# Kernel tuning notes

Measured on AMD Instinct MI355X. Metric: run time of the kernel, lower is better.

The kernel has to match this reference:

```python
import jax, jax.numpy as jnp
import numpy as np

IN_DIM = 128
NUM_IDX = 128
LATENT = 512
FF_HID = 4 * IN_DIM
EPS = 1e-5


def _layernorm(x, g, b):
    mu = jnp.mean(x, axis=-1, keepdims=True)
    var = jnp.mean((x - mu) ** 2, axis=-1, keepdims=True)
    return (x - mu) * jax.lax.rsqrt(var + EPS) * g + b


def setup_inputs() -> dict:
    key = jax.random.key(0)
    ks = jax.random.split(key, 12)
    B, N, D, L = 16, NUM_IDX, IN_DIM, LATENT
    s = lambda fan_in: 1.0 / np.sqrt(fan_in)
    return {
        "in_obs": jax.random.normal(ks[0], (B, N, D), jnp.float32),
        "Wq_w": jax.random.normal(ks[1], (D, L), jnp.float32) * s(D),
        "Wq_b": jax.random.normal(ks[2], (L,), jnp.float32) * s(D),
        "Wk_w": jax.random.normal(ks[3], (D, L), jnp.float32) * s(D),
        "Wk_b": jax.random.normal(ks[4], (L,), jnp.float32) * s(D),
        "wv_w": jax.random.normal(ks[5], (2 * L + 2 * N,), jnp.float32) * s(2 * L + 2 * N),
        "wv_b": jax.random.normal(ks[6], (), jnp.float32) * s(2 * L + 2 * N),
        "g1": jnp.ones((D,), jnp.float32),
        "b1": jnp.zeros((D,), jnp.float32),
        "ff1_w": jax.random.normal(ks[7], (D, FF_HID), jnp.float32) * s(D),
        "ff1_b": jax.random.normal(ks[8], (FF_HID,), jnp.float32) * s(D),
        "ff2_w": jax.random.normal(ks[9], (FF_HID, D), jnp.float32) * s(FF_HID),
        "ff2_b": jax.random.normal(ks[10], (D,), jnp.float32) * s(FF_HID),
        "g2": jnp.ones((D,), jnp.float32),
        "b2": jnp.zeros((D,), jnp.float32),
    }


def reference(in_obs, Wq_w, Wq_b, Wk_w, Wk_b, wv_w, wv_b, g1, b1,
              ff1_w, ff1_b, ff2_w, ff2_b, g2, b2):
    # in_obs: [B, N, D]
    B, N, D = in_obs.shape
    L = Wq_w.shape[1]
    eye = jnp.broadcast_to(jnp.eye(N, dtype=in_obs.dtype), (B, N, N))
    # q_cat/k_cat: [B, N, L+N]
    q_cat = jnp.concatenate([in_obs @ Wq_w + Wq_b, eye], axis=-1)
    k_cat = jnp.concatenate([in_obs @ Wk_w + Wk_b, eye], axis=-1)
    # Original: w_v(tanh(concat(q_i, k_j))). tanh is elementwise and the dot
    # product splits over the concat, so score[b,i,j] = a[b,i] + c[b,j] + bias
    # -- mathematically identical, avoids the [B,N,N,2L+2N] intermediate.
    a = jnp.tanh(q_cat) @ wv_w[: L + N]          # [B, N]
    c = jnp.tanh(k_cat) @ wv_w[L + N:]           # [B, N]
    scores = a[:, :, None] + c[:, None, :] + wv_b  # [B, N, N]
    weights = jax.nn.softmax(scores, axis=-1)
    attn = weights @ in_obs                       # [B, N, D]
    res = _layernorm(attn + in_obs, g1, b1)
    ff = jax.nn.relu(res @ ff1_w + ff1_b) @ ff2_w + ff2_b
    return _layernorm(ff + in_obs, g2, b2)
```

## Files before the change

### kernel.cpp

```cpp
#include <hip/hip_runtime.h>

#define NN 128
#define DD 128
#define LL 512
#define FFH 512
#define TANH1 0.76159415595576489f

typedef __attribute__((ext_vector_type(8))) short bf16x8;
typedef __attribute__((ext_vector_type(4))) float f32x4;

struct alignas(16) f4arr { float v[4]; };

__device__ __forceinline__ unsigned short f2bf(float f) {
    union { float f; unsigned u; } v; v.f = f;
    return (unsigned short)((v.u + 0x7FFFu + ((v.u >> 16) & 1u)) >> 16);
}

__global__ __launch_bounds__(256) void kA(
    const float* __restrict__ in_obs,
    const float* __restrict__ Wk_w,
    const float* __restrict__ Wk_b,
    const float* __restrict__ wv_w,
    const float* __restrict__ ff1_w,
    const float* __restrict__ ff2_w,
    float* __restrict__ c_out,
    unsigned short* __restrict__ W1f,
    unsigned short* __restrict__ W2f)
{
    const int t = threadIdx.x;
    const int wave = t >> 6, lane = t & 63;

    if (blockIdx.x >= 256) {
        const int bi = blockIdx.x - 256;
        const int fg = bi & 127;
        const int jp = t >> 6;
        const int l15 = lane & 15, l4 = lane >> 4;
        const int j = jp * 2;
        unsigned short v0, v1;
        unsigned short* dst;
        if (bi < 128) {
            const int ks = fg & 3, mt = fg >> 2;
            v0 = f2bf(ff1_w[(ks * 32 + l4 * 8 + j    ) * FFH + mt * 16 + l15]);
            v1 = f2bf(ff1_w[(ks * 32 + l4 * 8 + j + 1) * FFH + mt * 16 + l15]);
            dst = W1f;
        } else {
            const int ks = fg & 15, mt = fg >> 4;
            v0 = f2bf(ff2_w[(ks * 32 + l4 * 8 + j    ) * DD + mt * 16 + l15]);
            v1 = f2bf(ff2_w[(ks * 32 + l4 * 8 + j + 1) * DD + mt * 16 + l15]);
            dst = W2f;
        }
        *(unsigned*)&dst[(fg * 64 + lane) * 8 + j] = (unsigned)v0 | ((unsigned)v1 << 16);
        return;
    }

    __shared__ float row_lds[8][128];
    __shared__ float red[8][4];
    const int row0 = blockIdx.x * 8;
    const float* src = in_obs + row0 * DD;
    #pragma unroll
    for (int i = 0; i < 4; ++i) {
        int idx = t + i * 256;
        row_lds[idx >> 7][idx & 127] = src[idx];
    }
    __syncthreads();

    const int l0 = t, l1 = t + 256;
    float acc0[8], acc1[8];
    #pragma unroll
    for (int r = 0; r < 8; ++r) { acc0[r] = 0.f; acc1[r] = 0.f; }

    #pragma unroll 4
    for (int d = 0; d < 128; d += 4) {
        f4arr rbuf[8];
        #pragma unroll
        for (int r = 0; r < 8; ++r)
            rbuf[r] = *(const f4arr*)&row_lds[r][d];
        #pragma unroll
        for (int dd = 0; dd < 4; ++dd) {
            const float w0 = Wk_w[(d + dd) * LL + l0];
            const float w1 = Wk_w[(d + dd) * LL + l1];
            #pragma unroll
            for (int r = 0; r < 8; ++r) {
                acc0[r] += rbuf[r].v[dd] * w0;
                acc1[r] += rbuf[r].v[dd] * w1;
            }
        }
    }
    const float kb0 = Wk_b[l0], kb1 = Wk_b[l1];
    const float wv0 = wv_w[640 + l0], wv1 = wv_w[640 + l1];
    float v[8];
    #pragma unroll
    for (int r = 0; r < 8; ++r)
        v[r] = tanhf(acc0[r] + kb0) * wv0 + tanhf(acc1[r] + kb1) * wv1;
    #pragma unroll
    for (int off = 32; off > 0; off >>= 1) {
        #pragma unroll
        for (int r = 0; r < 8; ++r)
            v[r] += __shfl_down(v[r], off, 64);
    }
    if (lane == 0) {
        #pragma unroll
        for (int r = 0; r < 8; ++r) red[r][wave] = v[r];
    }
    __syncthreads();
    if (t < 8) {
        const int row = row0 + t;
        const int j = row & (NN - 1);
        c_out[row] = red[t][0] + red[t][1] + red[t][2] + red[t][3]
                   + TANH1 * wv_w[1152 + j];
    }
}

__global__ __launch_bounds__(512, 2) void kB(
    const float* __restrict__ in_obs,
    const float* __restrict__ c_in,
    const unsigned short* __restrict__ W1f,
    const unsigned short* __restrict__ W2f,
    const float* __restrict__ g1, const float* __restrict__ b1,
    const float* __restrict__ ff1_b,
    const float* __restrict__ ff2_b,
    const float* __restrict__ g2, const float* __restrict__ b2,
    float* __restrict__ out)
{
    const int t = threadIdx.x;
    const int b = blockIdx.x >> 4;
    const int j0 = (blockIdx.x & 15) * 8;
    const int wave = t >> 6, lane = t & 63;
    const int l15 = lane & 15, l4 = lane >> 4;

    __shared__ float part[8][128];
    __shared__ alignas(16) unsigned short res_lds[16 * 128];
    __shared__ alignas(16) unsigned short h_lds[16 * 512];
    __shared__ alignas(16) float o2_lds[16 * 128];

    bf16x8 a1p[16];
    #pragma unroll
    for (int i = 0; i < 4; ++i)
        #pragma unroll
        for (int ks = 0; ks < 4; ++ks)
            a1p[i * 4 + ks] =
                *(const bf16x8*)(W1f + (((wave * 4 + i) * 4 + ks) * 64 + lane) * 8);
    bf16x8 a2p[16];
    #pragma unroll
    for (int ks = 0; ks < 16; ++ks)
        a2p[ks] = *(const bf16x8*)(W2f + ((wave * 16 + ks) * 64 + lane) * 8);

    const float cv0 = c_in[b * NN + lane];
    const float cv1 = c_in[b * NN + lane + 64];
    float mx = fmaxf(cv0, cv1);
    #pragma unroll
    for (int off = 32; off > 0; off >>= 1) mx = fmaxf(mx, __shfl_xor(mx, off, 64));
    float e0 = __expf(cv0 - mx), e1 = __expf(cv1 - mx);
    float sm = e0 + e1;
    #pragma unroll
    for (int off = 32; off > 0; off >>= 1) sm += __shfl_xor(sm, off, 64);
    const float inv = 1.f / sm;
    e0 *= inv; e1 *= inv;

    {
        const float* base = in_obs + (b * NN + wave * 16) * DD;
        float a0 = 0.f, a1 = 0.f;
        #pragma unroll
        for (int jj = 0; jj < 16; ++jj) {
            const int js = wave * 16 + jj;
            const float wj = (wave < 4) ? __shfl(e0, js, 64)
                                        : __shfl(e1, js - 64, 64);
            a0 += wj * base[jj * DD + lane];
            a1 += wj * base[jj * DD + 64 + lane];
        }
        part[wave][lane] = a0;
        part[wave][lane + 64] = a1;
    }
    __syncthreads();

    {
        const int r = wave;
        const int row = b * NN + j0 + r;
        const int c0i = lane * 2;
        const float2 xo = *(const float2*)&in_obs[row * DD + c0i];
        float x0 = xo.x, x1 = xo.y;
        #pragma unroll
        for (int g = 0; g < 8; ++g) {
            const float2 p = *(const float2*)&part[g][c0i];
            x0 += p.x; x1 += p.y;
        }
        float s = x0 + x1;
        #pragma unroll
        for (int off = 32; off > 0; off >>= 1) s += __shfl_xor(s, off, 64);
        const float mu = s * (1.f / 128.f);
        const float d0 = x0 - mu, d1 = x1 - mu;
        float vs = d0 * d0 + d1 * d1;
        #pragma unroll
        for (int off = 32; off > 0; off >>= 1) vs += __shfl_xor(vs, off, 64);
        const float rstd = rsqrtf(vs * (1.f / 128.f) + 1e-5f);
        const float2 gv = *(const float2*)&g1[c0i];
        const float2 bv = *(const float2*)&b1[c0i];
        const float r0 = d0 * rstd * gv.x + bv.x;
        const float r1 = d1 * rstd * gv.y + bv.y;
        const unsigned pk = (unsigned)f2bf(r0) | ((unsigned)f2bf(r1) << 16);
        const int swz = (lane * 4) ^ ((r & 7) << 4);
        *(unsigned*)((char*)res_lds + r * 256 + swz) = pk;
        *(unsigned*)((char*)res_lds + (r + 8) * 256 + (lane * 4)) = 0u;
    }
    __syncthreads();

    {
        bf16x8 bfrag[4];
        #pragma unroll
        for (int ks = 0; ks < 4; ++ks) {
            const int off = l15 * 256 + ((ks * 64 + l4 * 16) ^ ((l15 & 7) << 4));
            bfrag[ks] = *(const bf16x8*)((const char*)res_lds + off);
        }
        #pragma unroll
        for (int i = 0; i < 4; ++i) {
            const int mt = wave * 4 + i;
            f32x4 acc = {0.f, 0.f, 0.f, 0.f};
            #pragma unroll
            for (int ks = 0; ks < 4; ++ks)
                acc = __builtin_amdgcn_mfma_f32_16x16x32_bf16(
                          a1p[i * 4 + ks], bfrag[ks], acc, 0, 0, 0);
            const f4arr bias = *(const f4arr*)&ff1_b[mt * 16 + l4 * 4];
            uint2 pk;
            pk.x = (unsigned)f2bf(fmaxf(acc[0] + bias.v[0], 0.f))
                 | ((unsigned)f2bf(fmaxf(acc[1] + bias.v[1], 0.f)) << 16);
            pk.y = (unsigned)f2bf(fmaxf(acc[2] + bias.v[2], 0.f))
                 | ((unsigned)f2bf(fmaxf(acc[3] + bias.v[3], 0.f)) << 16);
            const int off = l15 * 1024 + ((mt * 32 + l4 * 8) ^ ((l15 & 7) << 4));
            *(uint2*)((char*)h_lds + off) = pk;
        }
    }
    __syncthreads();

    {
        f32x4 acc = {0.f, 0.f, 0.f, 0.f};
        #pragma unroll
        for (int ks = 0; ks < 16; ++ks) {
            const int off = l15 * 1024 + ((ks * 64 + l4 * 16) ^ ((l15 & 7) << 4));
            const bf16x8 bfrag = *(const bf16x8*)((const char*)h_lds + off);
            acc = __builtin_amdgcn_mfma_f32_16x16x32_bf16(a2p[ks], bfrag, acc, 0, 0, 0);
        }
        const int off = l15 * 512 + ((wave * 64 + l4 * 16) ^ ((l15 & 7) << 4));
        *(f32x4*)((char*)o2_lds + off) = acc;
    }
    __syncthreads();

    {
        const int r = wave;
        const int row = b * NN + j0 + r;
        const int c0i = lane * 2;
        const int off = r * 512 + ((lane * 8) ^ ((r & 7) << 4));
        const float2 o2 = *(const float2*)((char*)o2_lds + off);
        const float2 fb = *(const float2*)&ff2_b[c0i];
        const float2 xo = *(const float2*)&in_obs[row * DD + c0i];
        const float f0 = o2.x + fb.x + xo.x;
        const float f1 = o2.y + fb.y + xo.y;
        float s = f0 + f1;
        #pragma unroll
        for (int off2 = 32; off2 > 0; off2 >>= 1) s += __shfl_xor(s, off2, 64);
        const float mu = s * (1.f / 128.f);
        const float d0 = f0 - mu, d1 = f1 - mu;
        float vs = d0 * d0 + d1 * d1;
        #pragma unroll
        for (int off2 = 32; off2 > 0; off2 >>= 1) vs += __shfl_xor(vs, off2, 64);
        const float rstd = rsqrtf(vs * (1.f / 128.f) + 1e-5f);
        const float2 gv = *(const float2*)&g2[c0i];
        const float2 bv = *(const float2*)&b2[c0i];
        float2 o;
        o.x = d0 * rstd * gv.x + bv.x;
        o.y = d1 * rstd * gv.y + bv.y;
        *(float2*)&out[row * DD + c0i] = o;
    }
}

extern "C" void kernel_launch(void* const* d_in, const int* in_sizes, int n_in,
                              void* d_out, int out_size, void* d_ws, size_t ws_size,
                              hipStream_t stream) {
    const float* in_obs = (const float*)d_in[0];
    const float* Wk_w  = (const float*)d_in[3];
    const float* Wk_b  = (const float*)d_in[4];
    const float* wv_w  = (const float*)d_in[5];
    const float* g1    = (const float*)d_in[7];
    const float* b1    = (const float*)d_in[8];
    const float* ff1_w = (const float*)d_in[9];
    const float* ff1_b = (const float*)d_in[10];
    const float* ff2_w = (const float*)d_in[11];
    const float* ff2_b = (const float*)d_in[12];
    const float* g2    = (const float*)d_in[13];
    const float* b2    = (const float*)d_in[14];
    float* outp = (float*)d_out;

    unsigned short* W1f = (unsigned short*)d_ws;
    unsigned short* W2f = W1f + 65536;
    float* c_ws = (float*)((char*)d_ws + 262144);

    kA<<<512, 256, 0, stream>>>(in_obs, Wk_w, Wk_b, wv_w, ff1_w, ff2_w,
                                c_ws, W1f, W2f);
    kB<<<256, 512, 0, stream>>>(in_obs, c_ws, W1f, W2f, g1, b1,
                                ff1_b, ff2_b, g2, b2, outp);
}
```

Measured before the change: 25.90 us.

## Fuse key-score and FFN kernels into one, computing scores with bf16 MFMA

Merges the two launches into a single kernel. Each block now recomputes the key projection for its whole batch using bf16 MFMA from an LDS-staged bf16 copy of in_obs, with a fast exp-based tanh. FFN weights are converted to bf16 fragments on the fly from global fp32 memory instead of being pre-packed by a separate pass. This removes one launch and the workspace round trip, but the key projection is repeated 16 times per batch and each block does strided fp32 weight gathers. LDS use grows by 32 KB for in_frag, and the score path moves from fp32 to bf16.

```diff
diff --git a/kernel.cpp b/kernel.cpp
--- a/kernel.cpp
+++ b/kernel.cpp
@@ -16,106 +16,31 @@
     return (unsigned short)((v.u + 0x7FFFu + ((v.u >> 16) & 1u)) >> 16);
 }
 
-__global__ __launch_bounds__(256) void kA(
+__device__ __forceinline__ float tanh_fast(float x) {
+    const float e = __expf(2.f * x);
+    return 1.f - 2.f / (e + 1.f);
+}
+
+__device__ __forceinline__ bf16x8 gather_frag(const float* __restrict__ W,
+                                              int ld, int ks, int l4, int col) {
+    float x[8];
+    #pragma unroll
+    for (int je = 0; je < 8; ++je)
+        x[je] = W[(ks * 32 + l4 * 8 + je) * ld + col];
+    union { bf16x8 v; unsigned u[4]; } r;
+    #pragma unroll
+    for (int i = 0; i < 4; ++i)
+        r.u[i] = (unsigned)f2bf(x[2 * i]) | ((unsigned)f2bf(x[2 * i + 1]) << 16);
+    return r.v;
+}
+
+__global__ __launch_bounds__(512, 2) void k_all(
     const float* __restrict__ in_obs,
     const float* __restrict__ Wk_w,
     const float* __restrict__ Wk_b,
     const float* __restrict__ wv_w,
     const float* __restrict__ ff1_w,
     const float* __restrict__ ff2_w,
-    float* __restrict__ c_out,
-    unsigned short* __restrict__ W1f,
-    unsigned short* __restrict__ W2f)
-{
-    const int t = threadIdx.x;
-    const int wave = t >> 6, lane = t & 63;
-
-    if (blockIdx.x >= 256) {
-        const int bi = blockIdx.x - 256;
-        const int fg = bi & 127;
-        const int jp = t >> 6;
-        const int l15 = lane & 15, l4 = lane >> 4;
-        const int j = jp * 2;
-        unsigned short v0, v1;
-        unsigned short* dst;
-        if (bi < 128) {
-            const int ks = fg & 3, mt = fg >> 2;
-            v0 = f2bf(ff1_w[(ks * 32 + l4 * 8 + j    ) * FFH + mt * 16 + l15]);
-            v1 = f2bf(ff1_w[(ks * 32 + l4 * 8 + j + 1) * FFH + mt * 16 + l15]);
-            dst = W1f;
-        } else {
-            const int ks = fg & 15, mt = fg >> 4;
-            v0 = f2bf(ff2_w[(ks * 32 + l4 * 8 + j    ) * DD + mt * 16 + l15]);
-            v1 = f2bf(ff2_w[(ks * 32 + l4 * 8 + j + 1) * DD + mt * 16 + l15]);
-            dst = W2f;
-        }
-        *(unsigned*)&dst[(fg * 64 + lane) * 8 + j] = (unsigned)v0 | ((unsigned)v1 << 16);
-        return;
-    }
-
-    __shared__ float row_lds[8][128];
-    __shared__ float red[8][4];
-    const int row0 = blockIdx.x * 8;
-    const float* src = in_obs + row0 * DD;
-    #pragma unroll
-    for (int i = 0; i < 4; ++i) {
-        int idx = t + i * 256;
-        row_lds[idx >> 7][idx & 127] = src[idx];
-    }
-    __syncthreads();
-
-    const int l0 = t, l1 = t + 256;
-    float acc0[8], acc1[8];
-    #pragma unroll
-    for (int r = 0; r < 8; ++r) { acc0[r] = 0.f; acc1[r] = 0.f; }
-
-    #pragma unroll 4
-    for (int d = 0; d < 128; d += 4) {
-        f4arr rbuf[8];
-        #pragma unroll
-        for (int r = 0; r < 8; ++r)
-            rbuf[r] = *(const f4arr*)&row_lds[r][d];
-        #pragma unroll
-        for (int dd = 0; dd < 4; ++dd) {
-            const float w0 = Wk_w[(d + dd) * LL + l0];
-            const float w1 = Wk_w[(d + dd) * LL + l1];
-            #pragma unroll
-            for (int r = 0; r < 8; ++r) {
-                acc0[r] += rbuf[r].v[dd] * w0;
-                acc1[r] += rbuf[r].v[dd] * w1;
-            }
-        }
-    }
-    const float kb0 = Wk_b[l0], kb1 = Wk_b[l1];
-    const float wv0 = wv_w[640 + l0], wv1 = wv_w[640 + l1];
-    float v[8];
-    #pragma unroll
-    for (int r = 0; r < 8; ++r)
-        v[r] = tanhf(acc0[r] + kb0) * wv0 + tanhf(acc1[r] + kb1) * wv1;
-    #pragma unroll
-    for (int off = 32; off > 0; off >>= 1) {
-        #pragma unroll
-        for (int r = 0; r < 8; ++r)
-            v[r] += __shfl_down(v[r], off, 64);
-    }
-    if (lane == 0) {
-        #pragma unroll
-        for (int r = 0; r < 8; ++r) red[r][wave] = v[r];
-    }
-    __syncthreads();
-    if (t < 8) {
-        const int row = row0 + t;
-        const int j = row & (NN - 1);
-        c_out[row] = red[t][0] + red[t][1] + red[t][2] + red[t][3]
-                   + TANH1 * wv_w[1152 + j];
-    }
-}
-
-__global__ __launch_bounds__(512, 2) void kB(
-    const float* __restrict__ in_obs,
-    const float* __restrict__ c_in,
-    const unsigned short* __restrict__ W1f,
-    const unsigned short* __restrict__ W2f,
     const float* __restrict__ g1, const float* __restrict__ b1,
     const float* __restrict__ ff1_b,
     const float* __restrict__ ff2_b,
@@ -128,25 +53,86 @@
     const int wave = t >> 6, lane = t & 63;
     const int l15 = lane & 15, l4 = lane >> 4;
 
+    __shared__ alignas(16) unsigned short in_frag[128 * 128];
     __shared__ float part[8][128];
+    __shared__ float c_lds[128];
     __shared__ alignas(16) unsigned short res_lds[16 * 128];
     __shared__ alignas(16) unsigned short h_lds[16 * 512];
     __shared__ alignas(16) float o2_lds[16 * 128];
 
-    bf16x8 a1p[16];
-    #pragma unroll
-    for (int i = 0; i < 4; ++i)
-        #pragma unroll
-        for (int ks = 0; ks < 4; ++ks)
-            a1p[i * 4 + ks] =
-                *(const bf16x8*)(W1f + (((wave * 4 + i) * 4 + ks) * 64 + lane) * 8);
-    bf16x8 a2p[16];
-    #pragma unroll
-    for (int ks = 0; ks < 16; ++ks)
-        a2p[ks] = *(const bf16x8*)(W2f + ((wave * 16 + ks) * 64 + lane) * 8);
-
-    const float cv0 = c_in[b * NN + lane];
-    const float cv1 = c_in[b * NN + lane + 64];
+    {
+        const int r = t >> 2;
+        const int c0 = (t & 3) * 32;
+        const float* src = in_obs + (b * NN + r) * DD + c0;
+        const int swz = (r & 7) << 4;
+        #pragma unroll
+        for (int i = 0; i < 8; ++i) {
+            const float4 v = *(const float4*)(src + i * 4);
+            const unsigned p0 = (unsigned)f2bf(v.x) | ((unsigned)f2bf(v.y) << 16);
+            const unsigned p1 = (unsigned)f2bf(v.z) | ((unsigned)f2bf(v.w) << 16);
+            const int byte0 = (c0 + i * 4) * 2;
+            *(unsigned*)((char*)in_frag + r * 256 + (byte0 ^ swz)) = p0;
+            *(unsigned*)((char*)in_frag + r * 256 + ((byte0 + 4) ^ swz)) = p1;
+        }
+    }
+    __syncthreads();
+
+    float cj[8];
+    #pragma unroll
+    for (int mt = 0; mt < 8; ++mt) cj[mt] = 0.f;
+    {
+        bf16x8 aW[4][4];
+        #pragma unroll
+        for (int ni = 0; ni < 4; ++ni) {
+            const int ncol = (wave * 4 + ni) * 16 + l15;
+            #pragma unroll
+            for (int ks = 0; ks < 4; ++ks)
+                aW[ni][ks] = gather_frag(Wk_w, LL, ks, l4, ncol);
+        }
+        #pragma unroll
+        for (int mt = 0; mt < 8; ++mt) {
+            const int row = mt * 16 + l15;
+            bf16x8 bX[4];
+            #pragma unroll
+            for (int ks = 0; ks < 4; ++ks)
+                bX[ks] = *(const bf16x8*)((const char*)in_frag + row * 256
+                              + ((ks * 64 + l4 * 16) ^ ((row & 7) << 4)));
+            #pragma unroll
+            for (int ni = 0; ni < 4; ++ni) {
+                f32x4 acc = {0.f, 0.f, 0.f, 0.f};
+                #pragma unroll
+                for (int ks = 0; ks < 4; ++ks)
+                    acc = __builtin_amdgcn_mfma_f32_16x16x32_bf16(aW[ni][ks], bX[ks], acc, 0, 0, 0);
+                const int lb = (wave * 4 + ni) * 16 + l4 * 4;
+                const f4arr kb4 = *(const f4arr*)&Wk_b[lb];
+                const f4arr wv4 = *(const f4arr*)&wv_w[640 + lb];
+                #pragma unroll
+                for (int r = 0; r < 4; ++r)
+                    cj[mt] += tanh_fast(acc[r] + kb4.v[r]) * wv4.v[r];
+            }
+        }
+    }
+    #pragma unroll
+    for (int mt = 0; mt < 8; ++mt) {
+        cj[mt] += __shfl_xor(cj[mt], 16, 64);
+        cj[mt] += __shfl_xor(cj[mt], 32, 64);
+    }
+    if (lane < 16) {
+        #pragma unroll
+        for (int mt = 0; mt < 8; ++mt)
+            part[wave][mt * 16 + lane] = cj[mt];
+    }
+    __syncthreads();
+    if (t < 128) {
+        float cc = TANH1 * wv_w[1152 + t];
+        #pragma unroll
+        for (int g = 0; g < 8; ++g) cc += part[g][t];
+        c_lds[t] = cc;
+    }
+    __syncthreads();
+
+    const float cv0 = c_lds[lane];
+    const float cv1 = c_lds[lane + 64];
     float mx = fmaxf(cv0, cv1);
     #pragma unroll
     for (int off = 32; off > 0; off >>= 1) mx = fmaxf(mx, __shfl_xor(mx, off, 64));
@@ -216,9 +202,10 @@
             const int mt = wave * 4 + i;
             f32x4 acc = {0.f, 0.f, 0.f, 0.f};
             #pragma unroll
-            for (int ks = 0; ks < 4; ++ks)
-                acc = __builtin_amdgcn_mfma_f32_16x16x32_bf16(
-                          a1p[i * 4 + ks], bfrag[ks], acc, 0, 0, 0);
+            for (int ks = 0; ks < 4; ++ks) {
+                const bf16x8 afrag = gather_frag(ff1_w, FFH, ks, l4, mt * 16 + l15);
+                acc = __builtin_amdgcn_mfma_f32_16x16x32_bf16(afrag, bfrag[ks], acc, 0, 0, 0);
+            }
             const f4arr bias = *(const f4arr*)&ff1_b[mt * 16 + l4 * 4];
             uint2 pk;
             pk.x = (unsigned)f2bf(fmaxf(acc[0] + bias.v[0], 0.f))
@@ -237,7 +224,8 @@
         for (int ks = 0; ks < 16; ++ks) {
             const int off = l15 * 1024 + ((ks * 64 + l4 * 16) ^ ((l15 & 7) << 4));
             const bf16x8 bfrag = *(const bf16x8*)((const char*)h_lds + off);
-            acc = __builtin_amdgcn_mfma_f32_16x16x32_bf16(a2p[ks], bfrag, acc, 0, 0, 0);
+            const bf16x8 afrag = gather_frag(ff2_w, DD, ks, l4, wave * 16 + l15);
+            acc = __builtin_amdgcn_mfma_f32_16x16x32_bf16(afrag, bfrag, acc, 0, 0, 0);
         }
         const int off = l15 * 512 + ((wave * 64 + l4 * 16) ^ ((l15 & 7) << 4));
         *(f32x4*)((char*)o2_lds + off) = acc;
@@ -289,12 +277,6 @@
     const float* b2    = (const float*)d_in[14];
     float* outp = (float*)d_out;
 
-    unsigned short* W1f = (unsigned short*)d_ws;
-    unsigned short* W2f = W1f + 65536;
-    float* c_ws = (float*)((char*)d_ws + 262144);
-
-    kA<<<512, 256, 0, stream>>>(in_obs, Wk_w, Wk_b, wv_w, ff1_w, ff2_w,
-                                c_ws, W1f, W2f);
-    kB<<<256, 512, 0, stream>>>(in_obs, c_ws, W1f, W2f, g1, b1,
-                                ff1_b, ff2_b, g2, b2, outp);
-}
+    k_all<<<256, 512, 0, stream>>>(in_obs, Wk_w, Wk_b, wv_w, ff1_w, ff2_w,
+                                   g1, b1, ff1_b, ff2_b, g2, b2, outp);
+}
```

Result: slower. 33.58 us (+29.7%).

## Drop weight pre-pack pass; gather and convert FF weights inside main kernel

Applied to the files above, without the earlier changes.

Removes the separate blocks that converted ff1/ff2 weights to bf16 MFMA-fragment layout in a workspace. The main kernel now reads the fp32 weights directly with strided gathers and converts them to bf16 right before each MFMA. Launch bounds are raised to 4 waves-per-EU since the preloaded register fragments are gone. This trades a global write/read round trip and a lighter first kernel for 256 blocks each issuing many uncoalesced strided fp32 loads (about 8 per fragment) on the critical path of the GEMMs.

```diff
diff --git a/kernel.cpp b/kernel.cpp
--- a/kernel.cpp
+++ b/kernel.cpp
@@ -16,45 +16,31 @@
     return (unsigned short)((v.u + 0x7FFFu + ((v.u >> 16) & 1u)) >> 16);
 }
 
-__global__ __launch_bounds__(256) void kA(
+__device__ __forceinline__ bf16x8 gather_frag(const float* __restrict__ W,
+                                              int ld, int ks, int l4, int col) {
+    float x[8];
+    #pragma unroll
+    for (int je = 0; je < 8; ++je)
+        x[je] = W[(ks * 32 + l4 * 8 + je) * ld + col];
+    union { bf16x8 v; unsigned u[4]; } r;
+    #pragma unroll
+    for (int i = 0; i < 4; ++i)
+        r.u[i] = (unsigned)f2bf(x[2 * i]) | ((unsigned)f2bf(x[2 * i + 1]) << 16);
+    return r.v;
+}
+
+__global__ __launch_bounds__(256) void kScores(
     const float* __restrict__ in_obs,
     const float* __restrict__ Wk_w,
     const float* __restrict__ Wk_b,
     const float* __restrict__ wv_w,
-    const float* __restrict__ ff1_w,
-    const float* __restrict__ ff2_w,
-    float* __restrict__ c_out,
-    unsigned short* __restrict__ W1f,
-    unsigned short* __restrict__ W2f)
+    float* __restrict__ c_out)
 {
     const int t = threadIdx.x;
     const int wave = t >> 6, lane = t & 63;
-
-    if (blockIdx.x >= 256) {
-        const int bi = blockIdx.x - 256;
-        const int fg = bi & 127;
-        const int jp = t >> 6;
-        const int l15 = lane & 15, l4 = lane >> 4;
-        const int j = jp * 2;
-        unsigned short v0, v1;
-        unsigned short* dst;
-        if (bi < 128) {
-            const int ks = fg & 3, mt = fg >> 2;
-            v0 = f2bf(ff1_w[(ks * 32 + l4 * 8 + j    ) * FFH + mt * 16 + l15]);
-            v1 = f2bf(ff1_w[(ks * 32 + l4 * 8 + j + 1) * FFH + mt * 16 + l15]);
-            dst = W1f;
-        } else {
-            const int ks = fg & 15, mt = fg >> 4;
-            v0 = f2bf(ff2_w[(ks * 32 + l4 * 8 + j    ) * DD + mt * 16 + l15]);
-            v1 = f2bf(ff2_w[(ks * 32 + l4 * 8 + j + 1) * DD + mt * 16 + l15]);
-            dst = W2f;
-        }
-        *(unsigned*)&dst[(fg * 64 + lane) * 8 + j] = (unsigned)v0 | ((unsigned)v1 << 16);
-        return;
-    }
-
     __shared__ float row_lds[8][128];
     __shared__ float red[8][4];
+
     const int row0 = blockIdx.x * 8;
     const float* src = in_obs + row0 * DD;
     #pragma unroll
@@ -111,11 +97,11 @@
     }
 }
 
-__global__ __launch_bounds__(512, 2) void kB(
+__global__ __launch_bounds__(512, 4) void kB(
     const float* __restrict__ in_obs,
     const float* __restrict__ c_in,
-    const unsigned short* __restrict__ W1f,
-    const unsigned short* __restrict__ W2f,
+    const float* __restrict__ ff1_w,
+    const float* __restrict__ ff2_w,
     const float* __restrict__ g1, const float* __restrict__ b1,
     const float* __restrict__ ff1_b,
     const float* __restrict__ ff2_b,
@@ -133,18 +119,6 @@
     __shared__ alignas(16) unsigned short h_lds[16 * 512];
     __shared__ alignas(16) float o2_lds[16 * 128];
 
-    bf16x8 a1p[16];
-    #pragma unroll
-    for (int i = 0; i < 4; ++i)
-        #pragma unroll
-        for (int ks = 0; ks < 4; ++ks)
-            a1p[i * 4 + ks] =
-                *(const bf16x8*)(W1f + (((wave * 4 + i) * 4 + ks) * 64 + lane) * 8);
-    bf16x8 a2p[16];
-    #pragma unroll
-    for (int ks = 0; ks < 16; ++ks)
-        a2p[ks] = *(const bf16x8*)(W2f + ((wave * 16 + ks) * 64 + lane) * 8);
-
     const float cv0 = c_in[b * NN + lane];
     const float cv1 = c_in[b * NN + lane + 64];
     float mx = fmaxf(cv0, cv1);
@@ -216,9 +190,10 @@
             const int mt = wave * 4 + i;
             f32x4 acc = {0.f, 0.f, 0.f, 0.f};
             #pragma unroll
-            for (int ks = 0; ks < 4; ++ks)
-                acc = __builtin_amdgcn_mfma_f32_16x16x32_bf16(
-                          a1p[i * 4 + ks], bfrag[ks], acc, 0, 0, 0);
+            for (int ks = 0; ks < 4; ++ks) {
+                const bf16x8 afrag = gather_frag(ff1_w, FFH, ks, l4, mt * 16 + l15);
+                acc = __builtin_amdgcn_mfma_f32_16x16x32_bf16(afrag, bfrag[ks], acc, 0, 0, 0);
+            }
             const f4arr bias = *(const f4arr*)&ff1_b[mt * 16 + l4 * 4];
             uint2 pk;
             pk.x = (unsigned)f2bf(fmaxf(acc[0] + bias.v[0], 0.f))
@@ -237,7 +212,8 @@
         for (int ks = 0; ks < 16; ++ks) {
             const int off = l15 * 1024 + ((ks * 64 + l4 * 16) ^ ((l15 & 7) << 4));
             const bf16x8 bfrag = *(const bf16x8*)((const char*)h_lds + off);
-            acc = __builtin_amdgcn_mfma_f32_16x16x32_bf16(a2p[ks], bfrag, acc, 0, 0, 0);
+            const bf16x8 afrag = gather_frag(ff2_w, DD, ks, l4, wave * 16 + l15);
+            acc = __builtin_amdgcn_mfma_f32_16x16x32_bf16(afrag, bfrag, acc, 0, 0, 0);
         }
         const int off = l15 * 512 + ((wave * 64 + l4 * 16) ^ ((l15 & 7) << 4));
         *(f32x4*)((char*)o2_lds + off) = acc;
@@ -289,12 +265,9 @@
     const float* b2    = (const float*)d_in[14];
     float* outp = (float*)d_out;
 
-    unsigned short* W1f = (unsigned short*)d_ws;
-    unsigned short* W2f = W1f + 65536;
-    float* c_ws = (float*)((char*)d_ws + 262144);
-
-    kA<<<512, 256, 0, stream>>>(in_obs, Wk_w, Wk_b, wv_w, ff1_w, ff2_w,
-                                c_ws, W1f, W2f);
-    kB<<<256, 512, 0, stream>>>(in_obs, c_ws, W1f, W2f, g1, b1,
+    float* c_ws = (float*)d_ws;
+
+    kScores<<<256, 256, 0, stream>>>(in_obs, Wk_w, Wk_b, wv_w, c_ws);
+    kB<<<256, 512, 0, stream>>>(in_obs, c_ws, ff1_w, ff2_w, g1, b1,
                                 ff1_b, ff2_b, g2, b2, outp);
 }
```

After: 29.46 us. +13.8%, slower.
